# Kernel tuning notes

Measured on AMD Instinct MI355X. Metric: run time of the kernel, lower is better.

## Reference

```python
import jax, jax.numpy as jnp
import numpy as np

N = 100000          # nodes
E = 1600000         # edges (avg degree 16)
DIN = 64
DOUT = 64
EXPERTS = 3
GATE_C = 4
TEMP = 101.0        # batch=0 < decay_lim: 100 - 0 + final_temperature(1.0)


def setup_inputs() -> dict:
    key = jax.random.key(0)
    ks = jax.random.split(key, 6)
    x = jax.random.normal(ks[0], (N, DIN), dtype=jnp.float32)
    edge_index = jax.random.randint(ks[1], (2, E), 0, N, dtype=jnp.int32)
    gate_features = jax.random.normal(ks[2], (N, GATE_C), dtype=jnp.float32)
    # per-expert GCN linear weights/bias (PyG GCNConv: lin then bias)
    W = jax.random.normal(ks[3], (EXPERTS, DIN, DOUT), dtype=jnp.float32) / np.sqrt(DIN).astype(np.float32)
    b = jnp.zeros((EXPERTS, DOUT), dtype=jnp.float32)
    # gating nn.Linear(gate_channels, experts, bias=False); stored as [GATE_C, EXPERTS] so y = gf @ Wg
    Wg = jax.random.normal(ks[4], (GATE_C, EXPERTS), dtype=jnp.float32) / np.sqrt(GATE_C).astype(np.float32)
    return {"x": x, "edge_index": edge_index, "gate_features": gate_features,
            "W": W, "b": b, "Wg": Wg}


def reference(x, edge_index, gate_features, W, b, Wg):
    n = x.shape[0]
    # --- GCN normalization with self-loops (PyG GCNConv defaults) ---
    loops = jnp.arange(n, dtype=edge_index.dtype)
    rows = jnp.concatenate([edge_index[0], loops])   # source nodes, [E+N]
    cols = jnp.concatenate([edge_index[1], loops])   # target nodes, [E+N]
    deg = jax.ops.segment_sum(jnp.ones(rows.shape, dtype=x.dtype), cols, num_segments=n)
    dinv = jnp.where(deg > 0, jax.lax.rsqrt(deg), 0.0)
    norm = dinv[rows] * dinv[cols]                   # [E+N]

    # --- gating network (softmax with decayed temperature) ---
    gate = jax.nn.softmax((gate_features @ Wg) / jnp.asarray(TEMP, x.dtype), axis=-1)  # [N, EXPERTS]

    # --- experts: GCN conv -> ReLU -> gate-weighted accumulation ---
    out = jnp.zeros((n, W.shape[-1]), dtype=x.dtype)
    for i in range(W.shape[0]):                      # small fixed expert count
        xw = x @ W[i]                                # [N, DOUT]
        msg = xw[rows] * norm[:, None]               # gather + scale, [E+N, DOUT]
        agg = jax.ops.segment_sum(msg, cols, num_segments=n) + b[i]
        out = out + gate[:, i:i + 1] * jax.nn.relu(agg)
    return out
```

## Files before the change

### kernel.cpp

```cpp
#include <hip/hip_runtime.h>
#include <hip/hip_bf16.h>

#define NN 100000
#define NE 1600000
#define NT 6250

#define NBUCK  511
#define BRANGE 196
#define CAPB   3584
#define CHUNK  4096
#define NCH    391

typedef __attribute__((ext_vector_type(8))) short bf16x8;
typedef __attribute__((ext_vector_type(4))) float f32x4;

__device__ inline float2 bf16x2_unpack(unsigned v) {
    float2 r;
    r.x = __uint_as_float(v << 16);
    r.y = __uint_as_float(v & 0xffff0000u);
    return r;
}
__device__ inline unsigned bf16x2_pack(float a, float b) {
    __hip_bfloat162 h2(__float2bfloat16(a), __float2bfloat16(b));
    unsigned u;
    __builtin_memcpy(&u, &h2, 4);
    return u;
}

__global__ __launch_bounds__(512) void binA_kernel(const int* __restrict__ cols,
                                                   int* __restrict__ hist_g) {
    __shared__ int hist[512];
    int t = threadIdx.x;
    int base = blockIdx.x * CHUNK;
    int cnt = min(CHUNK, NE - base);
    hist[t] = 0;
    __syncthreads();
    #pragma unroll
    for (int k = 0; k < CHUNK / 512; k++) {
        int i = k * 512 + t;
        if (i < cnt) atomicAdd(&hist[(unsigned)cols[base + i] / BRANGE], 1);
    }
    __syncthreads();
    hist_g[blockIdx.x * 512 + t] = hist[t];
}

__global__ __launch_bounds__(512) void scank_kernel(const int* __restrict__ hist_g,
                                                    int* __restrict__ gb,
                                                    int* __restrict__ cur,
                                                    const float* __restrict__ W,
                                                    __hip_bfloat16* __restrict__ Bp) {
    int t = threadIdx.x;
    if (blockIdx.x >= 32) {
        int idx = (blockIdx.x - 32) * 512 + t;
        if (idx < 12288) {
            int j    = idx & 7;
            int lane = (idx >> 3) & 63;
            int rest = idx >> 9;
            int tt   = rest % 12;
            int kh   = rest / 12;
            int k    = kh * 32 + (lane >> 4) * 8 + j;
            int col  = tt * 16 + (lane & 15);
            int i    = col >> 6;
            int d    = col & 63;
            Bp[idx] = __float2bfloat16(W[(i * 64 + k) * 64 + d]);
        }
        return;
    }
    int b = blockIdx.x * 16 + (t >> 5);
    int l = t & 31;
    int k0 = l * 13;
    int h[13];
    int s = 0;
    #pragma unroll
    for (int i = 0; i < 13; i++) {
        int k = k0 + i;
        h[i] = (k < NCH) ? hist_g[k * 512 + b] : 0;
        s += h[i];
    }
    int inc = s;
    #pragma unroll
    for (int off = 1; off < 32; off <<= 1) {
        int v = __shfl_up(inc, off);
        if (l >= off) inc += v;
    }
    int run = inc - s;
    #pragma unroll
    for (int i = 0; i < 13; i++) {
        int k = k0 + i;
        if (k < NCH) { gb[k * 512 + b] = run; run += h[i]; }
    }
    if (l == 31) cur[b * 16] = inc;
}

__global__ __launch_bounds__(1024) void binB_kernel(const int* __restrict__ rows,
                                                    const int* __restrict__ cols,
                                                    const int* __restrict__ hist_g,
                                                    const int* __restrict__ gb,
                                                    unsigned* __restrict__ eb) {
    __shared__ int excl[512];
    __shared__ int lcur[512];
    __shared__ int gbase[512];
    __shared__ unsigned staged[CHUNK];
    __shared__ unsigned short bktarr[CHUNK];
    int t = threadIdx.x;
    int base = blockIdx.x * CHUNK;
    int cnt = min(CHUNK, NE - base);

    int cbuf[CHUNK / 1024];
    int rbuf[CHUNK / 1024];
    #pragma unroll
    for (int k = 0; k < CHUNK / 1024; k++) {
        int i = k * 1024 + t;
        cbuf[k] = (i < cnt) ? cols[base + i] : -1;
        rbuf[k] = (i < cnt) ? rows[base + i] : 0;
    }
    if (t < 512) gbase[t] = gb[blockIdx.x * 512 + t];
    if (t < 64) {
        int h[8];
        #pragma unroll
        for (int k2 = 0; k2 < 8; k2++) h[k2] = hist_g[blockIdx.x * 512 + k2 * 64 + t];
        int carry = 0;
        #pragma unroll
        for (int k2 = 0; k2 < 8; k2++) {
            int inc = h[k2];
            #pragma unroll
            for (int off = 1; off < 64; off <<= 1) {
                int v = __shfl_up(inc, off);
                if (t >= off) inc += v;
            }
            int e = k2 * 64 + t;
            int ex = carry + inc - h[k2];
            excl[e] = ex;
            lcur[e] = ex;
            carry += __shfl(inc, 63);
        }
    }
    __syncthreads();

    #pragma unroll
    for (int k = 0; k < CHUNK / 1024; k++) {
        int c = cbuf[k];
        if (c >= 0) {
            int bkt = (unsigned)c / BRANGE;
            int lp = atomicAdd(&lcur[bkt], 1);
            staged[lp] = ((unsigned)(c - bkt * BRANGE) << 24) | (unsigned)rbuf[k];
            bktarr[lp] = (unsigned short)bkt;
        }
    }
    __syncthreads();

    #pragma unroll
    for (int k = 0; k < CHUNK / 1024; k++) {
        int i = k * 1024 + t;
        if (i < cnt) {
            int bkt = bktarr[i];
            int pos = gbase[bkt] + (i - excl[bkt]);
            if (pos < CAPB) eb[(size_t)bkt * CAPB + pos] = staged[i];
        }
    }
}

__global__ __launch_bounds__(1024) void sortn_kernel(const int* __restrict__ cur,
                                                     const unsigned* __restrict__ eb,
                                                     int* __restrict__ srcs2,
                                                     int2* __restrict__ nsd) {
    __shared__ unsigned recs[CAPB];
    __shared__ unsigned srcl[CAPB];
    __shared__ int hist[256];
    __shared__ int lcur[256];
    int b = blockIdx.x, t = threadIdx.x;
    if (t < 256) hist[t] = 0;
    __syncthreads();
    int cnt = min(cur[b * 16], CAPB);
    const unsigned* seg = eb + (size_t)b * CAPB;
    for (int i = t; i < cnt; i += 1024) {
        unsigned r = seg[i];
        recs[i] = r;
        atomicAdd(&hist[r >> 24], 1);
    }
    __syncthreads();
    if (t < 64) {
        int e = t * 4;
        int h0 = hist[e], h1 = hist[e + 1], h2 = hist[e + 2], h3 = hist[e + 3];
        int lsum = h0 + h1 + h2 + h3;
        int inc = lsum;
        #pragma unroll
        for (int off = 1; off < 64; off <<= 1) {
            int v = __shfl_up(inc, off);
            if (t >= off) inc += v;
        }
        int ex = inc - lsum;
        int e0 = ex, e1 = ex + h0, e2 = e1 + h1, e3 = e2 + h2;
        lcur[e] = e0; lcur[e + 1] = e1; lcur[e + 2] = e2; lcur[e + 3] = e3;
        int n = b * BRANGE + e;
        if (e     < BRANGE && n     < NN) nsd[n]     = make_int2(e0, h0);
        if (e + 1 < BRANGE && n + 1 < NN) nsd[n + 1] = make_int2(e1, h1);
        if (e + 2 < BRANGE && n + 2 < NN) nsd[n + 2] = make_int2(e2, h2);
        if (e + 3 < BRANGE && n + 3 < NN) nsd[n + 3] = make_int2(e3, h3);
    }
    __syncthreads();
    for (int i = t; i < cnt; i += 1024) {
        unsigned r = recs[i];
        int p = atomicAdd(&lcur[r >> 24], 1);
        srcl[p] = r & 0xFFFFFFu;
    }
    __syncthreads();
    for (int i = t; i < cnt; i += 1024)
        srcs2[(size_t)b * CAPB + i] = (int)srcl[i];
}

__global__ __launch_bounds__(256) void xscale_kernel(const float* __restrict__ x,
                                                     const int2* __restrict__ nsd,
                                                     unsigned* __restrict__ xs) {
    int i = blockIdx.x * 256 + threadIdx.x;
    int n = i >> 5;
    int d = (i & 31) * 2;
    float2 v = *(const float2*)(x + (size_t)n * 64 + d);
    float dv = rsqrtf((float)(nsd[n].y + 1));
    xs[i] = bf16x2_pack(v.x * dv, v.y * dv);
}

__global__ __launch_bounds__(256) void gmm_kernel(const int* __restrict__ srcs2,
                                                  const int2* __restrict__ nsd,
                                                  const unsigned* __restrict__ xs,
                                                  const short* __restrict__ Bp,
                                                  const float* __restrict__ bias,
                                                  const float* __restrict__ gf,
                                                  const float* __restrict__ Wg,
                                                  float* __restrict__ out) {
    __shared__ unsigned atile[16][32];
    int lane = threadIdx.x & 63;
    int wave = threadIdx.x >> 6;
    int g  = lane >> 4;
    int gl = lane & 15;
    int gb = g << 4;
    int n0 = blockIdx.x * 16;

    int nl = wave * 4 + g;
    int n = n0 + nl;
    int2 sd = nsd[n];
    int deg = sd.y;
    int bkt = (unsigned)n / BRANGE;
    const int* seg = srcs2 + (size_t)bkt * CAPB + sd.x;
    const uint2* xsv = (const uint2*)xs;

    float4 acc = make_float4(0.f, 0.f, 0.f, 0.f);
    for (int base = 0; base < deg; base += 16) {
        int idx = 0;
        if (base + gl < deg) idx = seg[base + gl];
        int s0 = __shfl(idx, gb);
        uint2 v[16];
        #pragma unroll
        for (int j = 0; j < 16; j++) {
            int s = __shfl(idx, gb + j);
            s = (base + j < deg) ? s : s0;
            v[j] = xsv[(size_t)s * 16 + gl];
        }
        #pragma unroll
        for (int j = 0; j < 16; j++) {
            if (base + j < deg) {
                float2 f0 = bf16x2_unpack(v[j].x);
                float2 f1 = bf16x2_unpack(v[j].y);
                acc.x += f0.x; acc.y += f0.y;
                acc.z += f1.x; acc.w += f1.y;
            }
        }
    }
    uint2 svu = xsv[(size_t)n * 16 + gl];
    float2 sv0 = bf16x2_unpack(svu.x);
    float2 sv1 = bf16x2_unpack(svu.y);
    float dn = rsqrtf((float)(deg + 1));
    uint2 o;
    o.x = bf16x2_pack((acc.x + sv0.x) * dn, (acc.y + sv0.y) * dn);
    o.y = bf16x2_pack((acc.z + sv1.x) * dn, (acc.w + sv1.y) * dn);
    ((uint2*)atile[nl])[gl] = o;
    __syncthreads();

    int m = lane & 15, quad = lane >> 4;
    int dpos = wave;
    const bf16x8* arow = (const bf16x8*)atile[m];
    bf16x8 a0 = arow[quad];
    bf16x8 a1 = arow[quad + 4];

    f32x4 ce[3];
    #pragma unroll
    for (int e = 0; e < 3; e++) ce[e] = (f32x4)(0.0f);
    #pragma unroll
    for (int kh = 0; kh < 2; kh++) {
        bf16x8 a = kh ? a1 : a0;
        #pragma unroll
        for (int e = 0; e < 3; e++) {
            bf16x8 bf = *(const bf16x8*)(Bp + ((size_t)((kh * 12 + e * 4 + dpos) * 64 + lane)) * 8);
            ce[e] = __builtin_amdgcn_mfma_f32_16x16x32_bf16(a, bf, ce[e], 0, 0, 0);
        }
    }

    float wg[12];
    #pragma unroll
    for (int k = 0; k < 12; k++) wg[k] = Wg[k];

    int d = dpos * 16 + m;
    float b0 = bias[0 * 64 + d], b1 = bias[1 * 64 + d], b2 = bias[2 * 64 + d];
    #pragma unroll
    for (int reg = 0; reg < 4; reg++) {
        int nn = n0 + quad * 4 + reg;
        float4 gv = ((const float4*)gf)[nn];
        float l0 = (gv.x*wg[0] + gv.y*wg[3] + gv.z*wg[6] + gv.w*wg[9])  * (1.0f/101.0f);
        float l1 = (gv.x*wg[1] + gv.y*wg[4] + gv.z*wg[7] + gv.w*wg[10]) * (1.0f/101.0f);
        float l2 = (gv.x*wg[2] + gv.y*wg[5] + gv.z*wg[8] + gv.w*wg[11]) * (1.0f/101.0f);
        float mx = fmaxf(l0, fmaxf(l1, l2));
        float e0 = __expf(l0 - mx), e1 = __expf(l1 - mx), e2 = __expf(l2 - mx);
        float inv = 1.0f / (e0 + e1 + e2);
        float v0 = ce[0][reg] + b0;
        float v1 = ce[1][reg] + b1;
        float v2 = ce[2][reg] + b2;
        float ov = (e0 * fmaxf(v0, 0.f) + e1 * fmaxf(v1, 0.f) + e2 * fmaxf(v2, 0.f)) * inv;
        out[(size_t)nn * 64 + d] = ov;
    }
}

extern "C" void kernel_launch(void* const* d_in, const int* in_sizes, int n_in,
                              void* d_out, int out_size, void* d_ws, size_t ws_size,
                              hipStream_t stream) {
    const float* x  = (const float*)d_in[0];
    const int*   ei = (const int*)d_in[1];
    const float* gf = (const float*)d_in[2];
    const float* W  = (const float*)d_in[3];
    const float* b  = (const float*)d_in[4];
    const float* Wg = (const float*)d_in[5];
    float* out = (float*)d_out;
    const int* rows = ei;
    const int* cols = ei + NE;

    char* ws = (char*)d_ws;
    size_t off = 0;
    auto alloc = [&](size_t bytes) {
        char* p = ws + off;
        off = (off + bytes + 255) & ~(size_t)255;
        return p;
    };
    int*            cur   = (int*)alloc(512 * 16 * 4);
    int*            histg = (int*)alloc((size_t)NCH * 512 * 4);
    int*            gbg   = (int*)alloc((size_t)NCH * 512 * 4);
    unsigned*       eb    = (unsigned*)alloc((size_t)NBUCK * CAPB * 4);
    int*            srcs2 = (int*)alloc((size_t)NBUCK * CAPB * 4);
    int2*           nsd   = (int2*)alloc((size_t)NN * 8);
    unsigned*       xs    = (unsigned*)alloc((size_t)NN * 32 * 4);
    __hip_bfloat16* Bp    = (__hip_bfloat16*)alloc(12288 * 2);

    binA_kernel<<<NCH, 512, 0, stream>>>(cols, histg);
    scank_kernel<<<56, 512, 0, stream>>>(histg, gbg, cur, W, Bp);
    binB_kernel<<<NCH, 1024, 0, stream>>>(rows, cols, histg, gbg, eb);
    sortn_kernel<<<NBUCK, 1024, 0, stream>>>(cur, eb, srcs2, nsd);
    xscale_kernel<<<NN * 32 / 256, 256, 0, stream>>>(x, nsd, xs);
    gmm_kernel<<<NT, 256, 0, stream>>>(srcs2, nsd, xs, (const short*)Bp, b, gf, Wg, out);
}
```

Baseline: 160.8 us.

## Pad per-node edge lists to multiples of 16 and double binning chunk size

Each node's neighbor list in the sorted source array is padded to a multiple of 16 entries, filled with a sentinel index that points to an extra all-zero row appended to the scaled feature buffer. This lets the gather loop drop its per-element bounds checks and masking. Separately, the binning chunk size is doubled (1024-thread binA blocks, half as many chunks), which shrinks the histogram scan. Padding adds wasted gathers of the zero row (about 7.5 per node on average) and enlarges the srcs2 buffer.

```diff
diff --git a/kernel.cpp b/kernel.cpp
--- a/kernel.cpp
+++ b/kernel.cpp
@@ -8,8 +8,9 @@
 #define NBUCK  511
 #define BRANGE 196
 #define CAPB   3584
-#define CHUNK  4096
-#define NCH    391
+#define CAPP   6720
+#define CHUNK  8192
+#define NCH    196
 
 typedef __attribute__((ext_vector_type(8))) short bf16x8;
 typedef __attribute__((ext_vector_type(4))) float f32x4;
@@ -27,21 +28,21 @@
     return u;
 }
 
-__global__ __launch_bounds__(512) void binA_kernel(const int* __restrict__ cols,
-                                                   int* __restrict__ hist_g) {
+__global__ __launch_bounds__(1024) void binA_kernel(const int* __restrict__ cols,
+                                                    int* __restrict__ hist_g) {
     __shared__ int hist[512];
     int t = threadIdx.x;
     int base = blockIdx.x * CHUNK;
     int cnt = min(CHUNK, NE - base);
-    hist[t] = 0;
-    __syncthreads();
-    #pragma unroll
-    for (int k = 0; k < CHUNK / 512; k++) {
-        int i = k * 512 + t;
+    if (t < 512) hist[t] = 0;
+    __syncthreads();
+    #pragma unroll
+    for (int k = 0; k < CHUNK / 1024; k++) {
+        int i = k * 1024 + t;
         if (i < cnt) atomicAdd(&hist[(unsigned)cols[base + i] / BRANGE], 1);
     }
     __syncthreads();
-    hist_g[blockIdx.x * 512 + t] = hist[t];
+    if (t < 512) hist_g[blockIdx.x * 512 + t] = hist[t];
 }
 
 __global__ __launch_bounds__(512) void scank_kernel(const int* __restrict__ hist_g,
@@ -68,11 +69,11 @@
     }
     int b = blockIdx.x * 16 + (t >> 5);
     int l = t & 31;
-    int k0 = l * 13;
-    int h[13];
+    int k0 = l * 7;
+    int h[7];
     int s = 0;
     #pragma unroll
-    for (int i = 0; i < 13; i++) {
+    for (int i = 0; i < 7; i++) {
         int k = k0 + i;
         h[i] = (k < NCH) ? hist_g[k * 512 + b] : 0;
         s += h[i];
@@ -85,7 +86,7 @@
     }
     int run = inc - s;
     #pragma unroll
-    for (int i = 0; i < 13; i++) {
+    for (int i = 0; i < 7; i++) {
         int k = k0 + i;
         if (k < NCH) { gb[k * 512 + b] = run; run += h[i]; }
     }
@@ -165,11 +166,13 @@
                                                      int* __restrict__ srcs2,
                                                      int2* __restrict__ nsd) {
     __shared__ unsigned recs[CAPB];
-    __shared__ unsigned srcl[CAPB];
+    __shared__ unsigned srcl[CAPP];
     __shared__ int hist[256];
     __shared__ int lcur[256];
+    __shared__ int ptot_s;
     int b = blockIdx.x, t = threadIdx.x;
     if (t < 256) hist[t] = 0;
+    for (int i = t; i < CAPP; i += 1024) srcl[i] = (unsigned)NN;
     __syncthreads();
     int cnt = min(cur[b * 16], CAPB);
     const unsigned* seg = eb + (size_t)b * CAPB;
@@ -182,7 +185,9 @@
     if (t < 64) {
         int e = t * 4;
         int h0 = hist[e], h1 = hist[e + 1], h2 = hist[e + 2], h3 = hist[e + 3];
-        int lsum = h0 + h1 + h2 + h3;
+        int p0 = (h0 + 15) & ~15, p1 = (h1 + 15) & ~15;
+        int p2 = (h2 + 15) & ~15, p3 = (h3 + 15) & ~15;
+        int lsum = p0 + p1 + p2 + p3;
         int inc = lsum;
         #pragma unroll
         for (int off = 1; off < 64; off <<= 1) {
@@ -190,13 +195,14 @@
             if (t >= off) inc += v;
         }
         int ex = inc - lsum;
-        int e0 = ex, e1 = ex + h0, e2 = e1 + h1, e3 = e2 + h2;
+        int e0 = ex, e1 = ex + p0, e2 = e1 + p1, e3 = e2 + p2;
         lcur[e] = e0; lcur[e + 1] = e1; lcur[e + 2] = e2; lcur[e + 3] = e3;
         int n = b * BRANGE + e;
         if (e     < BRANGE && n     < NN) nsd[n]     = make_int2(e0, h0);
         if (e + 1 < BRANGE && n + 1 < NN) nsd[n + 1] = make_int2(e1, h1);
         if (e + 2 < BRANGE && n + 2 < NN) nsd[n + 2] = make_int2(e2, h2);
         if (e + 3 < BRANGE && n + 3 < NN) nsd[n + 3] = make_int2(e3, h3);
+        if (t == 63) ptot_s = inc;
     }
     __syncthreads();
     for (int i = t; i < cnt; i += 1024) {
@@ -205,15 +211,18 @@
         srcl[p] = r & 0xFFFFFFu;
     }
     __syncthreads();
-    for (int i = t; i < cnt; i += 1024)
-        srcs2[(size_t)b * CAPB + i] = (int)srcl[i];
+    int ptot = ptot_s;
+    for (int i = t; i < ptot; i += 1024)
+        srcs2[(size_t)b * CAPP + i] = (int)srcl[i];
 }
 
 __global__ __launch_bounds__(256) void xscale_kernel(const float* __restrict__ x,
                                                      const int2* __restrict__ nsd,
                                                      unsigned* __restrict__ xs) {
     int i = blockIdx.x * 256 + threadIdx.x;
+    if (i >= (NN + 1) * 32) return;
     int n = i >> 5;
+    if (n == NN) { xs[i] = 0u; return; }
     int d = (i & 31) * 2;
     float2 v = *(const float2*)(x + (size_t)n * 64 + d);
     float dv = rsqrtf((float)(nsd[n].y + 1));
@@ -240,30 +249,26 @@
     int n = n0 + nl;
     int2 sd = nsd[n];
     int deg = sd.y;
+    int dgp = (deg + 15) & ~15;
     int bkt = (unsigned)n / BRANGE;
-    const int* seg = srcs2 + (size_t)bkt * CAPB + sd.x;
+    const int* seg = srcs2 + (size_t)bkt * CAPP + sd.x;
     const uint2* xsv = (const uint2*)xs;
 
     float4 acc = make_float4(0.f, 0.f, 0.f, 0.f);
-    for (int base = 0; base < deg; base += 16) {
-        int idx = 0;
-        if (base + gl < deg) idx = seg[base + gl];
-        int s0 = __shfl(idx, gb);
+    for (int base = 0; base < dgp; base += 16) {
+        int idx = seg[base + gl];
         uint2 v[16];
         #pragma unroll
         for (int j = 0; j < 16; j++) {
             int s = __shfl(idx, gb + j);
-            s = (base + j < deg) ? s : s0;
             v[j] = xsv[(size_t)s * 16 + gl];
         }
         #pragma unroll
         for (int j = 0; j < 16; j++) {
-            if (base + j < deg) {
-                float2 f0 = bf16x2_unpack(v[j].x);
-                float2 f1 = bf16x2_unpack(v[j].y);
-                acc.x += f0.x; acc.y += f0.y;
-                acc.z += f1.x; acc.w += f1.y;
-            }
+            float2 f0 = bf16x2_unpack(v[j].x);
+            float2 f1 = bf16x2_unpack(v[j].y);
+            acc.x += f0.x; acc.y += f0.y;
+            acc.z += f1.x; acc.w += f1.y;
         }
     }
     uint2 svu = xsv[(size_t)n * 16 + gl];
@@ -343,15 +348,15 @@
     int*            histg = (int*)alloc((size_t)NCH * 512 * 4);
     int*            gbg   = (int*)alloc((size_t)NCH * 512 * 4);
     unsigned*       eb    = (unsigned*)alloc((size_t)NBUCK * CAPB * 4);
-    int*            srcs2 = (int*)alloc((size_t)NBUCK * CAPB * 4);
+    int*            srcs2 = (int*)alloc((size_t)NBUCK * CAPP * 4);
     int2*           nsd   = (int2*)alloc((size_t)NN * 8);
-    unsigned*       xs    = (unsigned*)alloc((size_t)NN * 32 * 4);
+    unsigned*       xs    = (unsigned*)alloc((size_t)(NN + 1) * 32 * 4);
     __hip_bfloat16* Bp    = (__hip_bfloat16*)alloc(12288 * 2);
 
-    binA_kernel<<<NCH, 512, 0, stream>>>(cols, histg);
+    binA_kernel<<<NCH, 1024, 0, stream>>>(cols, histg);
     scank_kernel<<<56, 512, 0, stream>>>(histg, gbg, cur, W, Bp);
     binB_kernel<<<NCH, 1024, 0, stream>>>(rows, cols, histg, gbg, eb);
     sortn_kernel<<<NBUCK, 1024, 0, stream>>>(cur, eb, srcs2, nsd);
-    xscale_kernel<<<NN * 32 / 256, 256, 0, stream>>>(x, nsd, xs);
+    xscale_kernel<<<((NN + 1) * 32 + 255) / 256, 256, 0, stream>>>(x, nsd, xs);
     gmm_kernel<<<NT, 256, 0, stream>>>(srcs2, nsd, xs, (const short*)Bp, b, gf, Wg, out);
 }
```

Result: no change. 158.7 us (-1.3%).
